# Kernel optimization log

Measured on AMD Instinct MI355X. Metric: run time of the kernel, lower is better.

The kernel has to match this reference:

```python
import jax, jax.numpy as jnp
import numpy as np

N_EMBD = 1024
N_HEAD = 16
HEAD = N_EMBD // N_HEAD


def setup_inputs() -> dict:
    key = jax.random.key(0)
    k1, k2, k3 = jax.random.split(key, 3)
    x = jax.random.normal(k1, (2, 2048, N_EMBD), dtype=jnp.float32)
    # torch Linear weight is [out, in]; store transposed for x @ W
    W_attn = jax.random.normal(k2, (N_EMBD, 3 * N_EMBD), dtype=jnp.float32) * (1.0 / np.sqrt(N_EMBD))
    W_proj = jax.random.normal(k3, (N_EMBD, N_EMBD), dtype=jnp.float32) * (1.0 / np.sqrt(N_EMBD))
    return {"x": x, "W_attn": W_attn, "W_proj": W_proj}


def reference(x, W_attn, W_proj):
    B, T, C = x.shape
    qkv = x @ W_attn  # [B,T,3C]
    q, k, v = jnp.split(qkv, 3, axis=-1)
    # [B,T,H,D] -> [B,H,T,D]
    q = q.reshape(B, T, N_HEAD, HEAD).transpose(0, 2, 1, 3)
    k = k.reshape(B, T, N_HEAD, HEAD).transpose(0, 2, 1, 3)
    v = v.reshape(B, T, N_HEAD, HEAD).transpose(0, 2, 1, 3)
    att = jnp.einsum('bhqd,bhkd->bhqk', q, k) * (1.0 / np.sqrt(HEAD))
    causal = jnp.tril(jnp.ones((T, T), dtype=bool))
    att = jnp.where(causal[None, None], att, jnp.float32(-jnp.inf))
    att = jax.nn.softmax(att, axis=-1)
    y = jnp.einsum('bhqk,bhkd->bhqd', att, v)
    y = y.transpose(0, 2, 1, 3).reshape(B, T, C)
    return y @ W_proj
```

## Files before the change

### kernel.cpp

```cpp
#include <hip/hip_runtime.h>

typedef unsigned short u16;
typedef __bf16 bf16x8 __attribute__((ext_vector_type(8)));
typedef float f32x4 __attribute__((ext_vector_type(4)));

#define BB 2
#define TT 2048
#define CC 1024
#define HH 16
#define DD 64
#define MM (BB*TT)

__device__ __forceinline__ u16 f2b(float f) {
    union { float f; unsigned int i; } a; a.f = f;
    unsigned int u = a.i;
    unsigned int r = (u + 0x7FFFu + ((u >> 16) & 1u)) >> 16;
    return (u16)r;
}
__device__ __forceinline__ u16 f2b_fast(float f) {
    union { float f; unsigned int i; } a; a.f = f;
    return (u16)((a.i + 0x8000u) >> 16);
}

__device__ __forceinline__ void gld16(const u16* g, u16* l) {
    __builtin_amdgcn_global_load_lds(
        (const __attribute__((address_space(1))) unsigned int*)g,
        (__attribute__((address_space(3))) unsigned int*)l, 16, 0, 0);
}

__global__ __launch_bounds__(256) void prep_k(const float* __restrict__ x,
                                              u16* __restrict__ xb,
                                              const float* __restrict__ Wa,
                                              u16* __restrict__ Wat,
                                              const float* __restrict__ Wp,
                                              u16* __restrict__ Wpt) {
    __shared__ u16 tile[64][65];
    const int b = blockIdx.x;
    const int tid = threadIdx.x;
    if (b < 4096) {
        int i = b * 256 + tid;
        float4 v = ((const float4*)x)[i];
        ushort4 o;
        o.x = f2b(v.x); o.y = f2b(v.y); o.z = f2b(v.z); o.w = f2b(v.w);
        ((ushort4*)xb)[i] = o;
        return;
    }
    const float* in; u16* out; int K, N, n0, k0;
    if (b < 4096 + 768) {
        int bb = b - 4096;
        in = Wa; out = Wat; K = 1024; N = 3072;
        n0 = (bb % 48) * 64; k0 = (bb / 48) * 64;
    } else {
        int bb = b - 4096 - 768;
        in = Wp; out = Wpt; K = 1024; N = 1024;
        n0 = (bb % 16) * 64; k0 = (bb / 16) * 64;
    }
    const int tx = tid & 63, ty = tid >> 6;
    for (int i = 0; i < 16; i++) {
        int row = ty + i * 4;
        tile[row][tx] = f2b(in[(size_t)(k0 + row) * N + n0 + tx]);
    }
    __syncthreads();
    for (int i = 0; i < 16; i++) {
        int row = ty + i * 4;
        out[(size_t)(n0 + row) * K + k0 + tx] = tile[tx][row];
    }
}

__global__ __launch_bounds__(256) void transpose_v_k(const u16* __restrict__ in,
                                                     u16* __restrict__ out) {
    __shared__ u16 tile[64][65];
    int t0 = blockIdx.x * 64, bh = blockIdx.y;
    const u16* src = in + (size_t)bh * TT * DD;
    u16* dst = out + (size_t)bh * DD * TT;
    int tx = threadIdx.x, ty = threadIdx.y;
    for (int i = 0; i < 16; i++) {
        int row = ty + i * 4;
        tile[row][tx] = src[(size_t)(t0 + row) * DD + tx];
    }
    __syncthreads();
    for (int i = 0; i < 16; i++) {
        int row = ty + i * 4;
        dst[(size_t)row * TT + t0 + tx] = tile[tx][row];
    }
}

template<int MODE>
__global__ __launch_bounds__(256) void gemm_k(const u16* __restrict__ A,
                                              const u16* __restrict__ Bt,
                                              u16* __restrict__ Cq,
                                              u16* __restrict__ Ck,
                                              u16* __restrict__ Cv,
                                              float* __restrict__ Cout,
                                              int N, int K) {
    __shared__ __attribute__((aligned(16))) u16 As[128 * 32];
    __shared__ __attribute__((aligned(16))) u16 Bs[128 * 32];
    const int tid  = threadIdx.x;
    const int lane = tid & 63, w = tid >> 6;
    const int wm = w >> 1, wn = w & 1;
    const int quad = lane >> 4, l16 = lane & 15;
    const int m0 = blockIdx.x * 128, n0 = blockIdx.y * 128;

    f32x4 acc[4][4];
    for (int mi = 0; mi < 4; mi++)
        for (int ni = 0; ni < 4; ni++)
            for (int e = 0; e < 4; e++) acc[mi][ni][e] = 0.f;

    for (int k0 = 0; k0 < K; k0 += 32) {
        for (int i = 0; i < 2; i++) {
            int c = tid + 256 * i;
            int row = c >> 2, col = (c & 3) * 8;
            const u16* srcA;
            if constexpr (MODE == 0) {
                srcA = A + (size_t)(m0 + row) * K + k0 + col;
            } else {
                int m = m0 + row;
                int b = m >> 11, t = m & 2047;
                int kk = k0 + col;
                int h = kk >> 6, d = kk & 63;
                srcA = A + ((size_t)(b * HH + h) * TT + t) * DD + d;
            }
            gld16(srcA, &As[c * 8]);
            gld16(Bt + (size_t)(n0 + row) * K + k0 + col, &Bs[c * 8]);
        }
        __syncthreads();
        bf16x8 af[4], bfm[4];
        for (int mi = 0; mi < 4; mi++)
            af[mi] = *(const bf16x8*)&As[(wm * 64 + mi * 16 + l16) * 32 + quad * 8];
        for (int ni = 0; ni < 4; ni++)
            bfm[ni] = *(const bf16x8*)&Bs[(wn * 64 + ni * 16 + l16) * 32 + quad * 8];
        for (int mi = 0; mi < 4; mi++)
            for (int ni = 0; ni < 4; ni++)
                acc[mi][ni] = __builtin_amdgcn_mfma_f32_16x16x32_bf16(
                    af[mi], bfm[ni], acc[mi][ni], 0, 0, 0);
        __syncthreads();
    }

    const float SCQ = 0.125f * 1.44269504f;
    for (int mi = 0; mi < 4; mi++)
        for (int ni = 0; ni < 4; ni++)
            for (int r = 0; r < 4; r++) {
                int row = m0 + wm * 64 + mi * 16 + quad * 4 + r;
                int col = n0 + wn * 64 + ni * 16 + l16;
                if constexpr (MODE == 0) {
                    int which = col >> 10;
                    int h = (col >> 6) & 15, d = col & 63;
                    int b = row >> 11, t = row & 2047;
                    size_t off = ((size_t)(b * HH + h) * TT + t) * DD + d;
                    float val = acc[mi][ni][r];
                    if (which == 0) val *= SCQ;
                    (which == 0 ? Cq : which == 1 ? Ck : Cv)[off] = f2b(val);
                } else {
                    Cout[(size_t)row * N + col] = acc[mi][ni][r];
                }
            }
}

__global__ __launch_bounds__(256, 2) void attn_k(const u16* __restrict__ Q,
                                                 const u16* __restrict__ Kb,
                                                 const u16* __restrict__ Vtg,
                                                 u16* __restrict__ Y) {
    __shared__ __attribute__((aligned(16))) u16 Ks[2][128 * 64];
    __shared__ __attribute__((aligned(16))) u16 Vs[2][64 * 128];
    __shared__ __attribute__((aligned(16))) u16 Ps[4][16 * 128];
    const int tid  = threadIdx.x;
    const int lane = tid & 63, w = tid >> 6;
    const int quad = lane >> 4, l16 = lane & 15;
    const int bh = blockIdx.x;
    const int y  = blockIdx.y;
    const int rowi = (y >> 1) & 3, coli = y >> 3;
    const int basew = ((coli & 1) ? 9 : 16) - ((coli >> 1) << 3);
    const int work = basew + ((coli & 1) ? rowi : -rowi);
    const int sb = 2 * (work - 1) + (y & 1);
    const int nkt = work;
    const size_t base  = (size_t)bh * TT * DD;
    const size_t baseV = (size_t)bh * DD * TT;

    int ksidx[4], koff[4], voff[4];
    for (int r = 0; r < 4; r++) {
        int sidx = r * 256 + tid;
        ksidx[r] = sidx;
        int kr = sidx >> 3, ksl = sidx & 7;
        koff[r] = kr * 64 + ((ksl ^ (kr & 7)) << 3);
        int vr = sidx >> 4, vsl = sidx & 15;
        voff[r] = vr * TT + ((vsl ^ (vr & 7)) << 3);
    }
    const u16* kg = Kb + base;
    const u16* vg = Vtg + baseV;

    for (int r = 0; r < 4; r++) gld16(kg + koff[r], &Ks[0][ksidx[r] * 8]);
    for (int r = 0; r < 4; r++) gld16(vg + voff[r], &Vs[0][ksidx[r] * 8]);

    bf16x8 qf[2];
    for (int kk = 0; kk < 2; kk++)
        qf[kk] = *(const bf16x8*)(Q + base +
            (size_t)(sb * 64 + w * 16 + l16) * DD + kk * 32 + quad * 8);

    const int swx = (l16 & 7);
    const int swk0 = ((quad ^ swx) << 3);
    const int swk1 = (((4 + quad) ^ swx) << 3);

    float mst[4], lst[4];
    f32x4 oacc[4];
    for (int r = 0; r < 4; r++) { mst[r] = -1e30f; lst[r] = 0.f; }
    for (int nd = 0; nd < 4; nd++)
        for (int e = 0; e < 4; e++) oacc[nd][e] = 0.f;

    for (int jk = 0; jk < nkt; jk++) {
        const int cb = jk & 1;
        __syncthreads();

        if (jk + 1 < nkt) {
            const u16* kn = kg + (size_t)(jk + 1) * (128 * DD);
            const u16* vn = vg + (size_t)(jk + 1) * 128;
            for (int r = 0; r < 4; r++)
                gld16(kn + koff[r], &Ks[cb ^ 1][ksidx[r] * 8]);
            for (int r = 0; r < 4; r++)
                gld16(vn + voff[r], &Vs[cb ^ 1][ksidx[r] * 8]);
        }

        f32x4 s[8];
        for (int ni = 0; ni < 8; ni++)
            for (int e = 0; e < 4; e++) s[ni][e] = 0.f;
        {
            bf16x8 kfa[8];
            for (int ni = 0; ni < 8; ni++)
                kfa[ni] = *(const bf16x8*)&Ks[cb][(ni * 16 + l16) * 64 + swk0];
            for (int ni = 0; ni < 8; ni++)
                s[ni] = __builtin_amdgcn_mfma_f32_16x16x32_bf16(
                    qf[0], kfa[ni], s[ni], 0, 0, 0);
        }
        {
            bf16x8 kfa[8];
            for (int ni = 0; ni < 8; ni++)
                kfa[ni] = *(const bf16x8*)&Ks[cb][(ni * 16 + l16) * 64 + swk1];
            for (int ni = 0; ni < 8; ni++)
                s[ni] = __builtin_amdgcn_mfma_f32_16x16x32_bf16(
                    qf[1], kfa[ni], s[ni], 0, 0, 0);
        }

        if (jk == (sb >> 1)) {
            int row0 = sb * 64 + w * 16 + quad * 4;
            int col0 = jk * 128 + l16;
            for (int ni = 0; ni < 8; ni++)
                for (int r = 0; r < 4; r++)
                    if (col0 + ni * 16 > row0 + r) s[ni][r] = -1e30f;
        }
        float alpha[4];
        for (int r = 0; r < 4; r++) {
            float mx = s[0][r];
            for (int ni = 1; ni < 8; ni++) mx = fmaxf(mx, s[ni][r]);
            for (int off = 8; off >= 1; off >>= 1)
                mx = fmaxf(mx, __shfl_xor(mx, off));
            float mn = fmaxf(mst[r], mx);
            alpha[r] = __builtin_amdgcn_exp2f(mst[r] - mn);
            mst[r] = mn;
        }
        float rs[4] = {0.f, 0.f, 0.f, 0.f};
        for (int ni = 0; ni < 8; ni++)
            for (int r = 0; r < 4; r++) {
                float pv = __builtin_amdgcn_exp2f(s[ni][r] - mst[r]);
                rs[r] += pv;
                int row = quad * 4 + r;
                int cg  = ni * 2 + (l16 >> 3);
                Ps[w][row * 128 + ((cg ^ row) << 3) + (l16 & 7)] = f2b_fast(pv);
            }
        for (int r = 0; r < 4; r++) {
            float sm = rs[r];
            for (int off = 8; off >= 1; off >>= 1)
                sm += __shfl_xor(sm, off);
            lst[r] = lst[r] * alpha[r] + sm;
            for (int nd = 0; nd < 4; nd++) oacc[nd][r] *= alpha[r];
        }

        for (int kk = 0; kk < 4; kk++) {
            const int swv = (((kk * 4 + quad) ^ swx) << 3);
            bf16x8 vfa[4];
            for (int nd = 0; nd < 4; nd++)
                vfa[nd] = *(const bf16x8*)&Vs[cb][(nd * 16 + l16) * 128 + swv];
            bf16x8 pf = *(const bf16x8*)&Ps[w][l16 * 128 +
                (((kk * 4 + quad) ^ l16) << 3)];
            for (int nd = 0; nd < 4; nd++)
                oacc[nd] = __builtin_amdgcn_mfma_f32_16x16x32_bf16(
                    pf, vfa[nd], oacc[nd], 0, 0, 0);
        }
    }

    for (int nd = 0; nd < 4; nd++)
        for (int r = 0; r < 4; r++) {
            int row = sb * 64 + w * 16 + quad * 4 + r;
            int col = nd * 16 + l16;
            Y[base + (size_t)row * DD + col] = f2b(oacc[nd][r] / lst[r]);
        }
}

extern "C" void kernel_launch(void* const* d_in, const int* in_sizes, int n_in,
                              void* d_out, int out_size, void* d_ws, size_t ws_size,
                              hipStream_t stream) {
    const float* x      = (const float*)d_in[0];
    const float* W_attn = (const float*)d_in[1];
    const float* W_proj = (const float*)d_in[2];
    float* out = (float*)d_out;

    u16* Wt_attn = (u16*)d_ws;
    u16* Wt_proj = Wt_attn + 3072 * 1024;
    u16* xb      = Wt_proj + 1024 * 1024;
    u16* q       = xb + (size_t)MM * CC;
    u16* k       = q + (size_t)32 * 2048 * 64;
    u16* v       = k + (size_t)32 * 2048 * 64;
    u16* y       = v + (size_t)32 * 2048 * 64;
    u16* vt      = xb;

    prep_k<<<dim3(4096 + 768 + 256), 256, 0, stream>>>(
        x, xb, W_attn, Wt_attn, W_proj, Wt_proj);
    gemm_k<0><<<dim3(MM / 128, 3072 / 128), 256, 0, stream>>>(
        xb, Wt_attn, q, k, v, nullptr, 3072, 1024);
    transpose_v_k<<<dim3(TT / 64, BB * HH), dim3(64, 4), 0, stream>>>(v, vt);
    attn_k<<<dim3(32, 32), 256, 0, stream>>>(q, k, vt, y);
    gemm_k<1><<<dim3(MM / 128, 1024 / 128), 256, 0, stream>>>(
        y, Wt_proj, nullptr, nullptr, nullptr, out, 1024, 1024);
}
```

Baseline: 198.2 us.

## Double-buffer GEMM LDS tiles and remap blocks with XCD-aware swizzle

The GEMM kernel now keeps two LDS buffers, so the global-to-LDS load for the next K slice is issued before the MFMA work on the current slice, and one barrier per iteration is dropped. The launch becomes a 1D grid, and block IDs are remapped so that consecutive blocks landing on the same XCD (round-robin over 8) cover neighbouring output tiles, which should improve L2 reuse. The cost is double the LDS footprint (32 KB), which may reduce occupancy, and the remap assumes the grid size is divisible by 8.

After: 194.1 us. -2.1%, faster.

```diff
diff --git a/kernel.cpp b/kernel.cpp
--- a/kernel.cpp
+++ b/kernel.cpp
@@ -93,48 +93,59 @@
                                               u16* __restrict__ Cv,
                                               float* __restrict__ Cout,
                                               int N, int K) {
-    __shared__ __attribute__((aligned(16))) u16 As[128 * 32];
-    __shared__ __attribute__((aligned(16))) u16 Bs[128 * 32];
+    __shared__ __attribute__((aligned(16))) u16 As[2][128 * 32];
+    __shared__ __attribute__((aligned(16))) u16 Bs[2][128 * 32];
     const int tid  = threadIdx.x;
     const int lane = tid & 63, w = tid >> 6;
     const int wm = w >> 1, wn = w & 1;
     const int quad = lane >> 4, l16 = lane & 15;
-    const int m0 = blockIdx.x * 128, n0 = blockIdx.y * 128;
+
+    const int nwg = gridDim.x, lin = blockIdx.x;
+    const int cpx = nwg >> 3;
+    const int sw  = (lin & 7) * cpx + (lin >> 3);
+    const int ncols = N >> 7;
+    const int m0 = (sw / ncols) * 128, n0 = (sw % ncols) * 128;
 
     f32x4 acc[4][4];
     for (int mi = 0; mi < 4; mi++)
         for (int ni = 0; ni < 4; ni++)
             for (int e = 0; e < 4; e++) acc[mi][ni][e] = 0.f;
 
-    for (int k0 = 0; k0 < K; k0 += 32) {
-        for (int i = 0; i < 2; i++) {
-            int c = tid + 256 * i;
-            int row = c >> 2, col = (c & 3) * 8;
-            const u16* srcA;
-            if constexpr (MODE == 0) {
-                srcA = A + (size_t)(m0 + row) * K + k0 + col;
-            } else {
-                int m = m0 + row;
-                int b = m >> 11, t = m & 2047;
-                int kk = k0 + col;
-                int h = kk >> 6, d = kk & 63;
-                srcA = A + ((size_t)(b * HH + h) * TT + t) * DD + d;
-            }
-            gld16(srcA, &As[c * 8]);
-            gld16(Bt + (size_t)(n0 + row) * K + k0 + col, &Bs[c * 8]);
-        }
+#define GSTAGE(BUF, K0)                                                   \
+    for (int i = 0; i < 2; i++) {                                         \
+        int c = tid + 256 * i;                                            \
+        int row = c >> 2, col = (c & 3) * 8;                              \
+        const u16* srcA;                                                  \
+        if constexpr (MODE == 0) {                                        \
+            srcA = A + (size_t)(m0 + row) * K + (K0) + col;               \
+        } else {                                                          \
+            int m = m0 + row;                                             \
+            int b = m >> 11, t = m & 2047;                                \
+            int kk = (K0) + col;                                          \
+            int h = kk >> 6, d = kk & 63;                                 \
+            srcA = A + ((size_t)(b * HH + h) * TT + t) * DD + d;          \
+        }                                                                 \
+        gld16(srcA, &As[BUF][c * 8]);                                     \
+        gld16(Bt + (size_t)(n0 + row) * K + (K0) + col, &Bs[BUF][c * 8]); \
+    }
+
+    GSTAGE(0, 0);
+    const int nk = K >> 5;
+    for (int jk = 0; jk < nk; jk++) {
+        const int cb = jk & 1;
         __syncthreads();
+        if (jk + 1 < nk) { GSTAGE(cb ^ 1, (jk + 1) * 32); }
         bf16x8 af[4], bfm[4];
         for (int mi = 0; mi < 4; mi++)
-            af[mi] = *(const bf16x8*)&As[(wm * 64 + mi * 16 + l16) * 32 + quad * 8];
+            af[mi] = *(const bf16x8*)&As[cb][(wm * 64 + mi * 16 + l16) * 32 + quad * 8];
         for (int ni = 0; ni < 4; ni++)
-            bfm[ni] = *(const bf16x8*)&Bs[(wn * 64 + ni * 16 + l16) * 32 + quad * 8];
+            bfm[ni] = *(const bf16x8*)&Bs[cb][(wn * 64 + ni * 16 + l16) * 32 + quad * 8];
         for (int mi = 0; mi < 4; mi++)
             for (int ni = 0; ni < 4; ni++)
                 acc[mi][ni] = __builtin_amdgcn_mfma_f32_16x16x32_bf16(
                     af[mi], bfm[ni], acc[mi][ni], 0, 0, 0);
-        __syncthreads();
-    }
+    }
+#undef GSTAGE
 
     const float SCQ = 0.125f * 1.44269504f;
     for (int mi = 0; mi < 4; mi++)
@@ -313,10 +324,10 @@
 
     prep_k<<<dim3(4096 + 768 + 256), 256, 0, stream>>>(
         x, xb, W_attn, Wt_attn, W_proj, Wt_proj);
-    gemm_k<0><<<dim3(MM / 128, 3072 / 128), 256, 0, stream>>>(
+    gemm_k<0><<<dim3((MM / 128) * (3072 / 128)), 256, 0, stream>>>(
         xb, Wt_attn, q, k, v, nullptr, 3072, 1024);
     transpose_v_k<<<dim3(TT / 64, BB * HH), dim3(64, 4), 0, stream>>>(v, vt);
     attn_k<<<dim3(32, 32), 256, 0, stream>>>(q, k, vt, y);
-    gemm_k<1><<<dim3(MM / 128, 1024 / 128), 256, 0, stream>>>(
+    gemm_k<1><<<dim3((MM / 128) * (1024 / 128)), 256, 0, stream>>>(
         y, Wt_proj, nullptr, nullptr, nullptr, out, 1024, 1024);
 }
```
